# Optimization experiments

Hardware: AMD Instinct MI355X
Metric: run time of the kernel (lower is better)

The kernel has to match this reference:

```python
import jax, jax.numpy as jnp
import numpy as np

D_MODEL = 1024
N_HEADS = 16
HEAD_DIM = D_MODEL // N_HEADS
SEQ_LEN = 2048
BATCH = 2
THETA = 10000.0


def _rope_tables(dim, seq_len, theta=THETA):
    freqs = 1.0 / theta ** (jnp.arange(0, dim, 2, dtype=jnp.float32) / dim)  # (dim/2,)
    t = jnp.arange(seq_len, dtype=jnp.float32)
    ang = jnp.outer(t, freqs)  # (S, dim/2)
    # interleave each freq twice to match the (-x_odd, x_even) rotation layout
    cos = jnp.repeat(jnp.cos(ang), 2, axis=-1)  # (S, dim)
    sin = jnp.repeat(jnp.sin(ang), 2, axis=-1)
    return cos, sin


def _apply_rope(x, cos, sin):
    # x: (B, S, H, D); cos/sin: (S, D)
    x_rot = jnp.stack([-x[..., 1::2], x[..., ::2]], axis=-1).reshape(x.shape)
    return x * cos[None, :, None, :] + x_rot * sin[None, :, None, :]


def setup_inputs() -> dict:
    key = jax.random.key(0)
    ks = jax.random.split(key, 9)
    s = 1.0 / np.sqrt(D_MODEL)
    return {
        "x": jax.random.normal(ks[0], (BATCH, SEQ_LEN, D_MODEL), dtype=jnp.float32),
        "wq": jax.random.normal(ks[1], (D_MODEL, D_MODEL), jnp.float32) * s,
        "bq": jnp.zeros((D_MODEL,), jnp.float32),
        "wk": jax.random.normal(ks[2], (D_MODEL, D_MODEL), jnp.float32) * s,
        "bk": jnp.zeros((D_MODEL,), jnp.float32),
        "wv": jax.random.normal(ks[3], (D_MODEL, D_MODEL), jnp.float32) * s,
        "bv": jnp.zeros((D_MODEL,), jnp.float32),
        "wo": jax.random.normal(ks[4], (D_MODEL, D_MODEL), jnp.float32) * s,
        "bo": jnp.zeros((D_MODEL,), jnp.float32),
    }


def reference(x, wq, bq, wk, bk, wv, bv, wo, bo):
    B, S, _ = x.shape
    cos, sin = _rope_tables(HEAD_DIM, S)
    # projections (torch Linear: x @ W^T + b)
    q = (x @ wq.T + bq).reshape(B, S, N_HEADS, HEAD_DIM)
    k = (x @ wk.T + bk).reshape(B, S, N_HEADS, HEAD_DIM)
    v = (x @ wv.T + bv).reshape(B, S, N_HEADS, HEAD_DIM)
    q = _apply_rope(q, cos, sin)
    k = _apply_rope(k, cos, sin)
    # attention: bhqd, bhkd -> bhqk
    scale = 1.0 / np.sqrt(HEAD_DIM)
    scores = jnp.einsum("bqhd,bkhd->bhqk", q, k) * scale
    attn = jax.nn.softmax(scores, axis=-1)
    out = jnp.einsum("bhqk,bkhd->bqhd", attn, v).reshape(B, S, D_MODEL)
    return out @ wo.T + bo
```

## Files before the change

### kernel.cpp

```cpp
#include <hip/hip_runtime.h>

typedef __attribute__((ext_vector_type(8))) __bf16 bf16x8;
typedef __attribute__((ext_vector_type(4))) __bf16 bf16x4;
typedef __attribute__((ext_vector_type(4))) float f32x4;
typedef __attribute__((ext_vector_type(16))) float f32x16;
typedef __attribute__((ext_vector_type(4))) int i32x4;
typedef __attribute__((ext_vector_type(4))) unsigned short ushort4v;

__device__ __forceinline__ unsigned short f2bf(float f) {
  unsigned u = __builtin_bit_cast(unsigned, f);
  u += 0x7fffu + ((u >> 16) & 1u);
  return (unsigned short)(u >> 16);
}

__device__ __forceinline__ unsigned cvt_pk_bf16(float lo, float hi) {
  unsigned r;
  asm("v_cvt_pk_bf16_f32 %0, %1, %2" : "=v"(r) : "v"(lo), "v"(hi));
  return r;
}

__device__ __forceinline__ void pl32swap(unsigned& a, unsigned& b) {
  asm("v_permlane32_swap_b32 %0, %1" : "+v"(a), "+v"(b));
}

__device__ __forceinline__ void gload16(const void* g, void* l) {
  __builtin_amdgcn_global_load_lds(
      (const __attribute__((address_space(1))) void*)g,
      (__attribute__((address_space(3))) void*)l, 16, 0, 0);
}

__global__ __launch_bounds__(256) void convert_k(
    const float* __restrict__ x, const float* __restrict__ wq,
    const float* __restrict__ wk, const float* __restrict__ wv,
    const float* __restrict__ wo,
    unsigned short* __restrict__ xb, unsigned short* __restrict__ wqkv,
    unsigned short* __restrict__ wob, float* cosT, float* sinT) {
  if (blockIdx.x >= 8192) {
    const int idx = (blockIdx.x - 8192) * 256 + threadIdx.x;
    const int s = idx >> 5, j = idx & 31;
    const float freq = powf(10000.f, -(float)(2 * j) * (1.f / 64.f));
    const float ang = (float)s * freq;
    cosT[idx] = cosf(ang);
    sinT[idx] = sinf(ang);
    return;
  }
  const size_t i = ((size_t)blockIdx.x * 256 + threadIdx.x) * 4;
  const float* src; unsigned short* dst; size_t off;
  if (i < 4194304)      { src = x;  dst = xb;              off = i; }
  else if (i < 5242880) { src = wq; dst = wqkv;            off = i - 4194304; }
  else if (i < 6291456) { src = wk; dst = wqkv + 1048576;  off = i - 5242880; }
  else if (i < 7340032) { src = wv; dst = wqkv + 2097152;  off = i - 6291456; }
  else                  { src = wo; dst = wob;             off = i - 7340032; }
  f32x4 v = *(const f32x4*)(src + off);
  ushort4v o;
  o[0] = f2bf(v[0]); o[1] = f2bf(v[1]); o[2] = f2bf(v[2]); o[3] = f2bf(v[3]);
  *(ushort4v*)(dst + off) = o;
}

template <int EPI>
__global__ __launch_bounds__(512) void gemm_bt_k(
    const unsigned short* __restrict__ A, const unsigned short* __restrict__ B,
    int M, int N, int K,
    unsigned short* __restrict__ Qr, unsigned short* __restrict__ Kr,
    unsigned short* __restrict__ Vt,
    const float* __restrict__ bq, const float* __restrict__ bk,
    const float* __restrict__ bvv,
    const float* __restrict__ cosT, const float* __restrict__ sinT,
    float* __restrict__ Cout, const float* __restrict__ bias) {
  __shared__ char smem[32768];
  const int t = threadIdx.x;
  const int wave = t >> 6, lane = t & 63;
  const int l15 = lane & 15, g = lane >> 4;
  const int cpx = (int)gridDim.x >> 3;
  const int wg = (blockIdx.x & 7) * cpx + (blockIdx.x >> 3);
  const int nt = N >> 7;
  const int mb = (wg / nt) << 7;
  const int nb = (wg % nt) << 7;
  const int wm = (wave >> 2) << 6;
  const int wn = (wave & 3) << 5;

  const f32x4 zv = {0.f, 0.f, 0.f, 0.f};
  f32x4 acc[4][2];
#pragma unroll
  for (int i = 0; i < 4; i++)
#pragma unroll
    for (int j = 0; j < 2; j++) acc[i][j] = zv;

  for (int kt = 0; kt < K; kt += 64) {
#pragma unroll
    for (int i = 0; i < 2; i++) {
      const int lin = t * 16 + i * 8192;
      const int r = lin >> 7;
      const int cb = (lin & 127) ^ ((r & 7) << 4);
      gload16((const char*)A + ((size_t)(mb + r) * K + kt) * 2 + cb,
              smem + i * 8192 + wave * 1024);
      gload16((const char*)B + ((size_t)(nb + r) * K + kt) * 2 + cb,
              smem + 16384 + i * 8192 + wave * 1024);
    }
    __syncthreads();

    bf16x8 af[4][2], bfr[2][2];
    const int sw = (l15 & 7) << 4;
#pragma unroll
    for (int mf = 0; mf < 4; mf++) {
      const int r = wm + mf * 16 + l15;
#pragma unroll
      for (int kf = 0; kf < 2; kf++)
        af[mf][kf] = *(const bf16x8*)(smem + r * 128 + ((kf * 64 + g * 16) ^ sw));
    }
#pragma unroll
    for (int nf = 0; nf < 2; nf++) {
      const int r2 = wn + nf * 16 + l15;
#pragma unroll
      for (int kf = 0; kf < 2; kf++)
        bfr[nf][kf] = *(const bf16x8*)(smem + 16384 + r2 * 128 + ((kf * 64 + g * 16) ^ sw));
    }
#pragma unroll
    for (int mf = 0; mf < 4; mf++)
#pragma unroll
      for (int nf = 0; nf < 2; nf++) {
        acc[mf][nf] = __builtin_amdgcn_mfma_f32_16x16x32_bf16(af[mf][0], bfr[nf][0], acc[mf][nf], 0, 0, 0);
        acc[mf][nf] = __builtin_amdgcn_mfma_f32_16x16x32_bf16(af[mf][1], bfr[nf][1], acc[mf][nf], 0, 0, 0);
      }
    __syncthreads();
  }

#pragma unroll
  for (int mf = 0; mf < 4; mf++) {
#pragma unroll
    for (int nf = 0; nf < 2; nf++) {
      const int row0 = mb + wm + mf * 16 + g * 4;
      const int col = nb + wn + nf * 16 + l15;
      if (EPI == 1) {
        const float bsv = bias[col];
#pragma unroll
        for (int r = 0; r < 4; r++)
          Cout[(size_t)(row0 + r) * N + col] = acc[mf][nf][r] + bsv;
      } else {
        const int region = col >> 10;
        const int cc = col & 1023;
        const int h = cc >> 6, d = cc & 63;
        const float bias_v = (region == 0 ? bq : (region == 1 ? bk : bvv))[cc];
        if (region < 2) {
          unsigned short* Ob = (region == 0 ? Qr : Kr);
          const float scl = (region == 0) ? 0.180336880111120425f : 1.0f;
#pragma unroll
          for (int r = 0; r < 4; r++) {
            const int row = row0 + r;
            const int s = row & 2047;
            const int b = row >> 11;
            const float v = acc[mf][nf][r] + bias_v;
            const float p = __shfl_xor(v, 1);
            const float c = cosT[s * 32 + (d >> 1)];
            const float sn = sinT[s * 32 + (d >> 1)];
            float o = (d & 1) ? (v * c + p * sn) : (v * c - p * sn);
            o *= scl;
            Ob[((size_t)(b * 16 + h) * 2048 + s) * 64 + d] = f2bf(o);
          }
        } else {
          ushort4v w;
#pragma unroll
          for (int r = 0; r < 4; r++) w[r] = f2bf(acc[mf][nf][r] + bias_v);
          const int s = row0 & 2047;
          const int b = row0 >> 11;
          *(ushort4v*)(Vt + ((size_t)(b * 16 + h) * 64 + d) * 2048 + s) = w;
        }
      }
    }
  }
}

__global__ __launch_bounds__(256, 4) void flash_k(
    const unsigned short* __restrict__ Qr, const unsigned short* __restrict__ Kr,
    const unsigned short* __restrict__ Vt, unsigned short* __restrict__ Op,
    float* __restrict__ Lp) {
  __shared__ char smem[32768];
  const int bid = blockIdx.x;
  const int bh = ((bid & 7) << 2) | ((bid >> 3) & 3);
  const int rest = bid >> 5;
  const int qt = rest & 15;
  const int ck = rest >> 4;
  const int kvb = ck << 10;
  const int t = threadIdx.x;
  const int wave = t >> 6, lane = t & 63;
  const int l31 = lane & 31, h32 = lane >> 5;
  const int q0 = qt * 128 + wave * 32;
  const unsigned short* Qb = Qr + ((size_t)bh * 2048 + q0) * 64;
  const char* Kb = (const char*)(Kr + (size_t)bh * 2048 * 64);
  const char* Vb = (const char*)(Vt + (size_t)bh * 64 * 2048);

  bf16x8 qB[4];
#pragma unroll
  for (int t4 = 0; t4 < 4; t4++)
    qB[t4] = *(const bf16x8*)(Qb + l31 * 64 + t4 * 16 + h32 * 8);

  const f32x16 z16 = {0,0,0,0,0,0,0,0,0,0,0,0,0,0,0,0};
  f32x16 ot0 = z16, ot1 = z16;
  float lsum = 0.f;
  const int swv = (l31 & 7) << 4;

#pragma unroll
  for (int i = 0; i < 2; i++) {
    const int lin = t * 16 + i * 4096;
    const int r = lin >> 7;
    const int cb = (lin & 127) ^ ((r & 7) << 4);
    gload16(Kb + (size_t)(kvb + r) * 128 + cb, smem + i * 4096 + wave * 1024);
    gload16(Vb + (size_t)r * 4096 + kvb * 2 + cb, smem + 8192 + i * 4096 + wave * 1024);
  }
  __syncthreads();

  for (int it = 0; it < 16; ++it) {
    const char* kb = smem + (it & 1) * 16384;
    const char* vbuf = kb + 8192;
    if (it < 15) {
      const int kvn = kvb + ((it + 1) << 6);
      char* kd = smem + ((it & 1) ^ 1) * 16384;
#pragma unroll
      for (int i = 0; i < 2; i++) {
        const int lin = t * 16 + i * 4096;
        const int r = lin >> 7;
        const int cb = (lin & 127) ^ ((r & 7) << 4);
        gload16(Kb + (size_t)(kvn + r) * 128 + cb, kd + i * 4096 + wave * 1024);
        gload16(Vb + (size_t)r * 4096 + kvn * 2 + cb, kd + 8192 + i * 4096 + wave * 1024);
      }
    }
    f32x16 st0 = z16, st1 = z16;
#pragma unroll
    for (int t4 = 0; t4 < 4; t4++) {
      const bf16x8 ka0 = *(const bf16x8*)(kb + l31 * 128 + ((t4 * 32 + h32 * 16) ^ swv));
      const bf16x8 ka1 = *(const bf16x8*)(kb + (32 + l31) * 128 + ((t4 * 32 + h32 * 16) ^ swv));
      st0 = __builtin_amdgcn_mfma_f32_32x32x16_bf16(ka0, qB[t4], st0, 0, 0, 0);
      st1 = __builtin_amdgcn_mfma_f32_32x32x16_bf16(ka1, qB[t4], st1, 0, 0, 0);
    }
    float ls0 = 0.f, ls1 = 0.f;
#pragma unroll
    for (int e = 0; e < 16; e++) {
      const float p0 = __builtin_amdgcn_exp2f(st0[e] - 16.0f);
      const float p1 = __builtin_amdgcn_exp2f(st1[e] - 16.0f);
      st0[e] = p0; st1[e] = p1;
      ls0 += p0; ls1 += p1;
    }
    lsum += ls0 + ls1;
#pragma unroll
    for (int tile = 0; tile < 2; tile++) {
      const f32x16& s = tile ? st1 : st0;
#pragma unroll
      for (int sg = 0; sg < 2; sg++) {
        unsigned b0 = cvt_pk_bf16(s[8 * sg + 0], s[8 * sg + 1]);
        unsigned b1 = cvt_pk_bf16(s[8 * sg + 2], s[8 * sg + 3]);
        unsigned b2 = cvt_pk_bf16(s[8 * sg + 4], s[8 * sg + 5]);
        unsigned b3 = cvt_pk_bf16(s[8 * sg + 6], s[8 * sg + 7]);
        pl32swap(b0, b2);
        pl32swap(b1, b3);
        const i32x4 bw = {(int)b0, (int)b1, (int)b2, (int)b3};
        const bf16x8 pb = __builtin_bit_cast(bf16x8, bw);
        const int kvbyte = tile * 64 + sg * 32 + h32 * 16;
        const bf16x8 va0 = *(const bf16x8*)(vbuf + l31 * 128 + (kvbyte ^ swv));
        const bf16x8 va1 = *(const bf16x8*)(vbuf + (32 + l31) * 128 + (kvbyte ^ swv));
        ot0 = __builtin_amdgcn_mfma_f32_32x32x16_bf16(va0, pb, ot0, 0, 0, 0);
        ot1 = __builtin_amdgcn_mfma_f32_32x32x16_bf16(va1, pb, ot1, 0, 0, 0);
      }
    }
    __syncthreads();
  }
  lsum += __shfl_xor(lsum, 32);
  const size_t obase = (((size_t)(ck * 32 + bh)) * 2048 + q0 + l31) * 64;
#pragma unroll
  for (int dt = 0; dt < 2; dt++) {
#pragma unroll
    for (int grp = 0; grp < 4; grp++) {
      bf16x4 w;
#pragma unroll
      for (int e = 0; e < 4; e++)
        w[e] = (__bf16)(dt ? ot1[grp * 4 + e] : ot0[grp * 4 + e]);
      *(bf16x4*)(Op + obase + dt * 32 + grp * 8 + 4 * h32) = w;
    }
  }
  if (lane < 32)
    Lp[((size_t)(ck * 32 + bh)) * 2048 + q0 + l31] = lsum;
}

__global__ __launch_bounds__(256) void reduce_k(
    const unsigned short* __restrict__ Op, const float* __restrict__ Lp,
    unsigned short* __restrict__ Oa) {
  const size_t o = ((size_t)blockIdx.x * 256 + threadIdx.x) * 8;
  const int d0 = (int)(o & 63);
  const int h  = (int)((o >> 6) & 15);
  const int s  = (int)((o >> 10) & 2047);
  const int b  = (int)(o >> 21);
  const size_t pi = (((size_t)(b * 16 + h)) * 2048 + s) * 64 + d0;
  const size_t li = ((size_t)(b * 16 + h)) * 2048 + s;
  const bf16x8 a = *(const bf16x8*)(Op + pi);
  const bf16x8 c = *(const bf16x8*)(Op + pi + 4194304);
  const float inv = 1.f / (Lp[li] + Lp[li + 65536]);
  bf16x8 w;
#pragma unroll
  for (int e = 0; e < 8; e++)
    w[e] = (__bf16)(((float)a[e] + (float)c[e]) * inv);
  *(bf16x8*)(Oa + o) = w;
}

extern "C" void kernel_launch(void* const* d_in, const int* in_sizes, int n_in,
                              void* d_out, int out_size, void* d_ws, size_t ws_size,
                              hipStream_t stream) {
  const float* x  = (const float*)d_in[0];
  const float* wq = (const float*)d_in[1];
  const float* bq = (const float*)d_in[2];
  const float* wk = (const float*)d_in[3];
  const float* bk = (const float*)d_in[4];
  const float* wv = (const float*)d_in[5];
  const float* bv = (const float*)d_in[6];
  const float* wo = (const float*)d_in[7];
  const float* bo = (const float*)d_in[8];
  float* out = (float*)d_out;
  char* ws = (char*)d_ws;

  unsigned short* xb    = (unsigned short*)(ws);
  unsigned short* wqkv  = (unsigned short*)(ws + 8388608);
  float* cosT           = (float*)(ws + 14680064);
  float* sinT           = (float*)(ws + 14942208);
  unsigned short* Opart = (unsigned short*)(ws);
  unsigned short* Qr    = (unsigned short*)(ws + 16777216);
  unsigned short* Oa    = (unsigned short*)(ws + 16777216);
  unsigned short* Kr    = (unsigned short*)(ws + 25165824);
  unsigned short* Vt    = (unsigned short*)(ws + 33554432);
  unsigned short* wob   = (unsigned short*)(ws + 41943040);
  float* Lpart          = (float*)(ws + 44040192);

  convert_k<<<dim3(8448), dim3(256), 0, stream>>>(x, wq, wk, wv, wo, xb, wqkv, wob, cosT, sinT);
  gemm_bt_k<0><<<dim3(32 * 24), dim3(512), 0, stream>>>(
      xb, wqkv, 4096, 3072, 1024, Qr, Kr, Vt, bq, bk, bv, cosT, sinT,
      (float*)nullptr, (const float*)nullptr);
  flash_k<<<dim3(1024), dim3(256), 0, stream>>>(Qr, Kr, Vt, Opart, Lpart);
  reduce_k<<<dim3(2048), dim3(256), 0, stream>>>(Opart, Lpart, Oa);
  gemm_bt_k<1><<<dim3(32 * 8), dim3(512), 0, stream>>>(
      Oa, wob, 4096, 1024, 1024,
      (unsigned short*)nullptr, (unsigned short*)nullptr, (unsigned short*)nullptr,
      (const float*)nullptr, (const float*)nullptr, (const float*)nullptr,
      cosT, sinT, out, bo);
}
```

Baseline: 119.2 us.

## Fuse split-KV partial reduction into output projection GEMM A-tile load

Removes the separate reduce kernel that combined the two flash-attention partial outputs and normalized by the summed softmax denominators. The output-projection GEMM now reads both partials and the L values directly while staging its A tile, combining and normalizing them in registers before writing to shared memory. This drops one launch and the write and re-read of the combined attention output. In exchange the A path uses synchronous vector loads plus arithmetic instead of async direct-to-LDS loads. Each partial element is also read once per N-tile block (8 times), not once.

```diff
diff --git a/kernel.cpp b/kernel.cpp
--- a/kernel.cpp
+++ b/kernel.cpp
@@ -66,7 +66,8 @@
     const float* __restrict__ bq, const float* __restrict__ bk,
     const float* __restrict__ bvv,
     const float* __restrict__ cosT, const float* __restrict__ sinT,
-    float* __restrict__ Cout, const float* __restrict__ bias) {
+    float* __restrict__ Cout, const float* __restrict__ bias,
+    const float* __restrict__ Lpar) {
   __shared__ char smem[32768];
   const int t = threadIdx.x;
   const int wave = t >> 6, lane = t & 63;
@@ -87,15 +88,37 @@
     for (int j = 0; j < 2; j++) acc[i][j] = zv;
 
   for (int kt = 0; kt < K; kt += 64) {
-#pragma unroll
-    for (int i = 0; i < 2; i++) {
-      const int lin = t * 16 + i * 8192;
-      const int r = lin >> 7;
-      const int cb = (lin & 127) ^ ((r & 7) << 4);
-      gload16((const char*)A + ((size_t)(mb + r) * K + kt) * 2 + cb,
-              smem + i * 8192 + wave * 1024);
-      gload16((const char*)B + ((size_t)(nb + r) * K + kt) * 2 + cb,
-              smem + 16384 + i * 8192 + wave * 1024);
+    if (EPI == 2) {
+      const int h = kt >> 6;
+      const size_t rowb = ((size_t)((mb >> 11) * 16 + h)) * 2048 + (mb & 2047);
+#pragma unroll
+      for (int i = 0; i < 2; i++) {
+        const int lin = t * 16 + i * 8192;
+        const int r = lin >> 7;
+        const int cb = (lin & 127) ^ ((r & 7) << 4);
+        const size_t row = rowb + r;
+        const bf16x8 a0 = *(const bf16x8*)((const char*)A + row * 128 + cb);
+        const bf16x8 a1 = *(const bf16x8*)((const char*)A + (row + 65536ull) * 128 + cb);
+        const float inv = 1.f / (Lpar[row] + Lpar[row + 65536]);
+        bf16x8 w;
+#pragma unroll
+        for (int e = 0; e < 8; e++)
+          w[e] = (__bf16)(((float)a0[e] + (float)a1[e]) * inv);
+        *(bf16x8*)(smem + lin) = w;
+        gload16((const char*)B + ((size_t)(nb + r) * K + kt) * 2 + cb,
+                smem + 16384 + i * 8192 + wave * 1024);
+      }
+    } else {
+#pragma unroll
+      for (int i = 0; i < 2; i++) {
+        const int lin = t * 16 + i * 8192;
+        const int r = lin >> 7;
+        const int cb = (lin & 127) ^ ((r & 7) << 4);
+        gload16((const char*)A + ((size_t)(mb + r) * K + kt) * 2 + cb,
+                smem + i * 8192 + wave * 1024);
+        gload16((const char*)B + ((size_t)(nb + r) * K + kt) * 2 + cb,
+                smem + 16384 + i * 8192 + wave * 1024);
+      }
     }
     __syncthreads();
 
@@ -131,7 +154,7 @@
     for (int nf = 0; nf < 2; nf++) {
       const int row0 = mb + wm + mf * 16 + g * 4;
       const int col = nb + wn + nf * 16 + l15;
-      if (EPI == 1) {
+      if (EPI != 0) {
         const float bsv = bias[col];
 #pragma unroll
         for (int r = 0; r < 4; r++)
@@ -280,26 +303,6 @@
     Lp[((size_t)(ck * 32 + bh)) * 2048 + q0 + l31] = lsum;
 }
 
-__global__ __launch_bounds__(256) void reduce_k(
-    const unsigned short* __restrict__ Op, const float* __restrict__ Lp,
-    unsigned short* __restrict__ Oa) {
-  const size_t o = ((size_t)blockIdx.x * 256 + threadIdx.x) * 8;
-  const int d0 = (int)(o & 63);
-  const int h  = (int)((o >> 6) & 15);
-  const int s  = (int)((o >> 10) & 2047);
-  const int b  = (int)(o >> 21);
-  const size_t pi = (((size_t)(b * 16 + h)) * 2048 + s) * 64 + d0;
-  const size_t li = ((size_t)(b * 16 + h)) * 2048 + s;
-  const bf16x8 a = *(const bf16x8*)(Op + pi);
-  const bf16x8 c = *(const bf16x8*)(Op + pi + 4194304);
-  const float inv = 1.f / (Lp[li] + Lp[li + 65536]);
-  bf16x8 w;
-#pragma unroll
-  for (int e = 0; e < 8; e++)
-    w[e] = (__bf16)(((float)a[e] + (float)c[e]) * inv);
-  *(bf16x8*)(Oa + o) = w;
-}
-
 extern "C" void kernel_launch(void* const* d_in, const int* in_sizes, int n_in,
                               void* d_out, int out_size, void* d_ws, size_t ws_size,
                               hipStream_t stream) {
@@ -321,7 +324,6 @@
   float* sinT           = (float*)(ws + 14942208);
   unsigned short* Opart = (unsigned short*)(ws);
   unsigned short* Qr    = (unsigned short*)(ws + 16777216);
-  unsigned short* Oa    = (unsigned short*)(ws + 16777216);
   unsigned short* Kr    = (unsigned short*)(ws + 25165824);
   unsigned short* Vt    = (unsigned short*)(ws + 33554432);
   unsigned short* wob   = (unsigned short*)(ws + 41943040);
@@ -330,12 +332,11 @@
   convert_k<<<dim3(8448), dim3(256), 0, stream>>>(x, wq, wk, wv, wo, xb, wqkv, wob, cosT, sinT);
   gemm_bt_k<0><<<dim3(32 * 24), dim3(512), 0, stream>>>(
       xb, wqkv, 4096, 3072, 1024, Qr, Kr, Vt, bq, bk, bv, cosT, sinT,
-      (float*)nullptr, (const float*)nullptr);
+      (float*)nullptr, (const float*)nullptr, (const float*)nullptr);
   flash_k<<<dim3(1024), dim3(256), 0, stream>>>(Qr, Kr, Vt, Opart, Lpart);
-  reduce_k<<<dim3(2048), dim3(256), 0, stream>>>(Opart, Lpart, Oa);
-  gemm_bt_k<1><<<dim3(32 * 8), dim3(512), 0, stream>>>(
-      Oa, wob, 4096, 1024, 1024,
+  gemm_bt_k<2><<<dim3(32 * 8), dim3(512), 0, stream>>>(
+      Opart, wob, 4096, 1024, 1024,
       (unsigned short*)nullptr, (unsigned short*)nullptr, (unsigned short*)nullptr,
       (const float*)nullptr, (const float*)nullptr, (const float*)nullptr,
-      cosT, sinT, out, bo);
-}
+      cosT, sinT, out, bo, Lpart);
+}
```

Measured after the change: 122.3 us. +2.6%, slower.

## Replace QKV projection GEMM with 256x256-tile double-buffered pipelined kernel

Applied to the files above, without the earlier changes.

Adds a new QKV projection kernel that uses 256x256 output tiles and 128KB of LDS double buffering. Global-to-LDS prefetch of the next k-step is interleaved with four MFMA phases per step, using explicit waitcnt, barriers and setprio. The larger tiles are meant to raise data reuse and hide load latency behind compute. In exchange the grid shrinks to 192 workgroups, fewer than the CU count, so some compute units may sit idle. The old templated GEMM keeps only the output-projection epilogue.

```diff
diff --git a/kernel.cpp b/kernel.cpp
--- a/kernel.cpp
+++ b/kernel.cpp
@@ -27,6 +27,11 @@
   __builtin_amdgcn_global_load_lds(
       (const __attribute__((address_space(1))) void*)g,
       (__attribute__((address_space(3))) void*)l, 16, 0, 0);
+}
+
+__device__ __forceinline__ void barrier_f() {
+  __builtin_amdgcn_s_barrier();
+  asm volatile("" ::: "memory");
 }
 
 __global__ __launch_bounds__(256) void convert_k(
@@ -55,6 +60,213 @@
   ushort4v o;
   o[0] = f2bf(v[0]); o[1] = f2bf(v[1]); o[2] = f2bf(v[2]); o[3] = f2bf(v[3]);
   *(ushort4v*)(dst + off) = o;
+}
+
+__device__ __forceinline__ void g256_stA(const unsigned short* A, int mb,
+                                         int kt, char* dbuf, int a, int t) {
+  const int row = a * 64 + (t >> 3);
+  const int cb = ((t & 7) * 16) ^ ((row & 7) << 4);
+  gload16((const char*)A + ((size_t)(mb + row) * 1024 + kt) * 2 + cb,
+          dbuf + a * 8192 + t * 16);
+}
+__device__ __forceinline__ void g256_stB(const unsigned short* B, int nb,
+                                         int kt, char* dbuf, int u, int v, int t) {
+  const int bu = (t >= 256) ? v : u;
+  const int tt = t & 255;
+  const int row = bu * 32 + (tt >> 3);
+  const int cb = ((tt & 7) * 16) ^ ((row & 7) << 4);
+  gload16((const char*)B + ((size_t)(nb + row) * 1024 + kt) * 2 + cb,
+          dbuf + 32768 + bu * 4096 + tt * 16);
+}
+
+template <bool PF>
+__device__ __forceinline__ void g256_kstep(
+    const unsigned short* __restrict__ A, const unsigned short* __restrict__ B,
+    int mb, int nb, int kt, char* smem, int l15, int g,
+    int wm, int wn, int t, f32x4 (&acc)[8][4]) {
+  const int d = (kt >> 6) & 1;
+  const char* Ab = smem + d * 65536;
+  const char* Bb = Ab + 32768;
+  char* sn = smem + (d ^ 1) * 65536;
+  const int kn = kt + 64;
+  const int sw = (l15 & 7) << 4;
+  bf16x8 af[4][2], bf[2][2];
+
+#pragma unroll
+  for (int mf = 0; mf < 4; mf++) {
+    const int r = wm + mf * 16 + l15;
+#pragma unroll
+    for (int kf = 0; kf < 2; kf++)
+      af[mf][kf] = *(const bf16x8*)(Ab + r * 128 + ((kf * 64 + g * 16) ^ sw));
+  }
+#pragma unroll
+  for (int nf = 0; nf < 2; nf++) {
+    const int r = wn + nf * 16 + l15;
+#pragma unroll
+    for (int kf = 0; kf < 2; kf++)
+      bf[nf][kf] = *(const bf16x8*)(Bb + r * 128 + ((kf * 64 + g * 16) ^ sw));
+  }
+  if (PF) { g256_stA(A, mb, kn, sn, 0, t); g256_stA(A, mb, kn, sn, 2, t); }
+  asm volatile("s_waitcnt lgkmcnt(0)" ::: "memory");
+  __builtin_amdgcn_sched_barrier(0);
+  __builtin_amdgcn_s_setprio(1);
+#pragma unroll
+  for (int mf = 0; mf < 4; mf++)
+#pragma unroll
+    for (int nf = 0; nf < 2; nf++) {
+      acc[mf][nf] = __builtin_amdgcn_mfma_f32_16x16x32_bf16(af[mf][0], bf[nf][0], acc[mf][nf], 0, 0, 0);
+      acc[mf][nf] = __builtin_amdgcn_mfma_f32_16x16x32_bf16(af[mf][1], bf[nf][1], acc[mf][nf], 0, 0, 0);
+    }
+  __builtin_amdgcn_s_setprio(0);
+  if (PF) { asm volatile("s_waitcnt vmcnt(4)" ::: "memory"); }
+  else    { asm volatile("s_waitcnt vmcnt(2)" ::: "memory"); }
+  barrier_f();
+
+#pragma unroll
+  for (int nf = 0; nf < 2; nf++) {
+    const int r = wn + 32 + nf * 16 + l15;
+#pragma unroll
+    for (int kf = 0; kf < 2; kf++)
+      bf[nf][kf] = *(const bf16x8*)(Bb + r * 128 + ((kf * 64 + g * 16) ^ sw));
+  }
+  if (PF) { g256_stB(B, nb, kn, sn, 0, 2, t); g256_stB(B, nb, kn, sn, 4, 6, t); }
+  asm volatile("s_waitcnt lgkmcnt(0)" ::: "memory");
+  __builtin_amdgcn_sched_barrier(0);
+  __builtin_amdgcn_s_setprio(1);
+#pragma unroll
+  for (int mf = 0; mf < 4; mf++)
+#pragma unroll
+    for (int nf = 0; nf < 2; nf++) {
+      acc[mf][2 + nf] = __builtin_amdgcn_mfma_f32_16x16x32_bf16(af[mf][0], bf[nf][0], acc[mf][2 + nf], 0, 0, 0);
+      acc[mf][2 + nf] = __builtin_amdgcn_mfma_f32_16x16x32_bf16(af[mf][1], bf[nf][1], acc[mf][2 + nf], 0, 0, 0);
+    }
+  __builtin_amdgcn_s_setprio(0);
+  if (PF) { asm volatile("s_waitcnt vmcnt(4)" ::: "memory"); }
+  else    { asm volatile("s_waitcnt vmcnt(0)" ::: "memory"); }
+  barrier_f();
+
+#pragma unroll
+  for (int mf = 0; mf < 4; mf++) {
+    const int r = wm + 64 + mf * 16 + l15;
+#pragma unroll
+    for (int kf = 0; kf < 2; kf++)
+      af[mf][kf] = *(const bf16x8*)(Ab + r * 128 + ((kf * 64 + g * 16) ^ sw));
+  }
+  if (PF) { g256_stB(B, nb, kn, sn, 1, 3, t); g256_stB(B, nb, kn, sn, 5, 7, t); }
+  asm volatile("s_waitcnt lgkmcnt(0)" ::: "memory");
+  __builtin_amdgcn_sched_barrier(0);
+  __builtin_amdgcn_s_setprio(1);
+#pragma unroll
+  for (int mf = 0; mf < 4; mf++)
+#pragma unroll
+    for (int nf = 0; nf < 2; nf++) {
+      acc[4 + mf][2 + nf] = __builtin_amdgcn_mfma_f32_16x16x32_bf16(af[mf][0], bf[nf][0], acc[4 + mf][2 + nf], 0, 0, 0);
+      acc[4 + mf][2 + nf] = __builtin_amdgcn_mfma_f32_16x16x32_bf16(af[mf][1], bf[nf][1], acc[4 + mf][2 + nf], 0, 0, 0);
+    }
+  __builtin_amdgcn_s_setprio(0);
+  barrier_f();
+
+#pragma unroll
+  for (int nf = 0; nf < 2; nf++) {
+    const int r = wn + nf * 16 + l15;
+#pragma unroll
+    for (int kf = 0; kf < 2; kf++)
+      bf[nf][kf] = *(const bf16x8*)(Bb + r * 128 + ((kf * 64 + g * 16) ^ sw));
+  }
+  if (PF) { g256_stA(A, mb, kn, sn, 1, t); g256_stA(A, mb, kn, sn, 3, t); }
+  asm volatile("s_waitcnt lgkmcnt(0)" ::: "memory");
+  __builtin_amdgcn_sched_barrier(0);
+  __builtin_amdgcn_s_setprio(1);
+#pragma unroll
+  for (int mf = 0; mf < 4; mf++)
+#pragma unroll
+    for (int nf = 0; nf < 2; nf++) {
+      acc[4 + mf][nf] = __builtin_amdgcn_mfma_f32_16x16x32_bf16(af[mf][0], bf[nf][0], acc[4 + mf][nf], 0, 0, 0);
+      acc[4 + mf][nf] = __builtin_amdgcn_mfma_f32_16x16x32_bf16(af[mf][1], bf[nf][1], acc[4 + mf][nf], 0, 0, 0);
+    }
+  __builtin_amdgcn_s_setprio(0);
+  if (PF) {
+    asm volatile("s_waitcnt vmcnt(4)" ::: "memory");
+    barrier_f();
+  }
+}
+
+__global__ __launch_bounds__(512, 2) void gemm256_k(
+    const unsigned short* __restrict__ A, const unsigned short* __restrict__ B,
+    unsigned short* __restrict__ Qr, unsigned short* __restrict__ Kr,
+    unsigned short* __restrict__ Vt,
+    const float* __restrict__ bq, const float* __restrict__ bk,
+    const float* __restrict__ bvv,
+    const float* __restrict__ cosT, const float* __restrict__ sinT) {
+  __shared__ char smem[131072];
+  const int t = threadIdx.x;
+  const int wave = t >> 6, lane = t & 63;
+  const int l15 = lane & 15, g = lane >> 4;
+  const int cpx = (int)gridDim.x >> 3;
+  const int wg = (blockIdx.x & 7) * cpx + (blockIdx.x >> 3);
+  const int mb = (wg / 12) << 8;
+  const int nb = (wg % 12) << 8;
+  const int wm = (wave >> 2) << 7;
+  const int wn = (wave & 3) << 6;
+
+  const f32x4 zv = {0.f, 0.f, 0.f, 0.f};
+  f32x4 acc[8][4];
+#pragma unroll
+  for (int i = 0; i < 8; i++)
+#pragma unroll
+    for (int j = 0; j < 4; j++) acc[i][j] = zv;
+
+  g256_stA(A, mb, 0, smem, 0, t);
+  g256_stA(A, mb, 0, smem, 2, t);
+  g256_stB(B, nb, 0, smem, 0, 2, t);
+  g256_stB(B, nb, 0, smem, 4, 6, t);
+  g256_stB(B, nb, 0, smem, 1, 3, t);
+  g256_stB(B, nb, 0, smem, 5, 7, t);
+  g256_stA(A, mb, 0, smem, 1, t);
+  g256_stA(A, mb, 0, smem, 3, t);
+  asm volatile("s_waitcnt vmcnt(4)" ::: "memory");
+  barrier_f();
+
+  for (int kt = 0; kt < 960; kt += 64)
+    g256_kstep<true>(A, B, mb, nb, kt, smem, l15, g, wm, wn, t, acc);
+  g256_kstep<false>(A, B, mb, nb, 960, smem, l15, g, wm, wn, t, acc);
+
+#pragma unroll
+  for (int MF = 0; MF < 8; MF++) {
+#pragma unroll
+    for (int NF = 0; NF < 4; NF++) {
+      const int row0 = mb + wm + MF * 16 + g * 4;
+      const int col = nb + wn + NF * 16 + l15;
+      const int region = col >> 10;
+      const int cc = col & 1023;
+      const int h = cc >> 6, dd = cc & 63;
+      const float bias_v = (region == 0 ? bq : (region == 1 ? bk : bvv))[cc];
+      if (region < 2) {
+        unsigned short* Ob = (region == 0 ? Qr : Kr);
+        const float scl = (region == 0) ? 0.180336880111120425f : 1.0f;
+#pragma unroll
+        for (int r = 0; r < 4; r++) {
+          const int row = row0 + r;
+          const int s = row & 2047;
+          const int b = row >> 11;
+          const float v = acc[MF][NF][r] + bias_v;
+          const float p = __shfl_xor(v, 1);
+          const float c = cosT[s * 32 + (dd >> 1)];
+          const float sn = sinT[s * 32 + (dd >> 1)];
+          float o = (dd & 1) ? (v * c + p * sn) : (v * c - p * sn);
+          o *= scl;
+          Ob[((size_t)(b * 16 + h) * 2048 + s) * 64 + dd] = f2bf(o);
+        }
+      } else {
+        ushort4v w;
+#pragma unroll
+        for (int r = 0; r < 4; r++) w[r] = f2bf(acc[MF][NF][r] + bias_v);
+        const int s = row0 & 2047;
+        const int b = row0 >> 11;
+        *(ushort4v*)(Vt + ((size_t)(b * 16 + h) * 64 + dd) * 2048 + s) = w;
+      }
+    }
+  }
 }
 
 template <int EPI>
@@ -131,41 +343,10 @@
     for (int nf = 0; nf < 2; nf++) {
       const int row0 = mb + wm + mf * 16 + g * 4;
       const int col = nb + wn + nf * 16 + l15;
-      if (EPI == 1) {
-        const float bsv = bias[col];
-#pragma unroll
-        for (int r = 0; r < 4; r++)
-          Cout[(size_t)(row0 + r) * N + col] = acc[mf][nf][r] + bsv;
-      } else {
-        const int region = col >> 10;
-        const int cc = col & 1023;
-        const int h = cc >> 6, d = cc & 63;
-        const float bias_v = (region == 0 ? bq : (region == 1 ? bk : bvv))[cc];
-        if (region < 2) {
-          unsigned short* Ob = (region == 0 ? Qr : Kr);
-          const float scl = (region == 0) ? 0.180336880111120425f : 1.0f;
-#pragma unroll
-          for (int r = 0; r < 4; r++) {
-            const int row = row0 + r;
-            const int s = row & 2047;
-            const int b = row >> 11;
-            const float v = acc[mf][nf][r] + bias_v;
-            const float p = __shfl_xor(v, 1);
-            const float c = cosT[s * 32 + (d >> 1)];
-            const float sn = sinT[s * 32 + (d >> 1)];
-            float o = (d & 1) ? (v * c + p * sn) : (v * c - p * sn);
-            o *= scl;
-            Ob[((size_t)(b * 16 + h) * 2048 + s) * 64 + d] = f2bf(o);
-          }
-        } else {
-          ushort4v w;
-#pragma unroll
-          for (int r = 0; r < 4; r++) w[r] = f2bf(acc[mf][nf][r] + bias_v);
-          const int s = row0 & 2047;
-          const int b = row0 >> 11;
-          *(ushort4v*)(Vt + ((size_t)(b * 16 + h) * 64 + d) * 2048 + s) = w;
-        }
-      }
+      const float bsv = bias[col];
+#pragma unroll
+      for (int r = 0; r < 4; r++)
+        Cout[(size_t)(row0 + r) * N + col] = acc[mf][nf][r] + bsv;
     }
   }
 }
@@ -328,9 +509,8 @@
   float* Lpart          = (float*)(ws + 44040192);
 
   convert_k<<<dim3(8448), dim3(256), 0, stream>>>(x, wq, wk, wv, wo, xb, wqkv, wob, cosT, sinT);
-  gemm_bt_k<0><<<dim3(32 * 24), dim3(512), 0, stream>>>(
-      xb, wqkv, 4096, 3072, 1024, Qr, Kr, Vt, bq, bk, bv, cosT, sinT,
-      (float*)nullptr, (const float*)nullptr);
+  gemm256_k<<<dim3(192), dim3(512), 0, stream>>>(
+      xb, wqkv, Qr, Kr, Vt, bq, bk, bv, cosT, sinT);
   flash_k<<<dim3(1024), dim3(256), 0, stream>>>(Qr, Kr, Vt, Opart, Lpart);
   reduce_k<<<dim3(2048), dim3(256), 0, stream>>>(Opart, Lpart, Oa);
   gemm_bt_k<1><<<dim3(32 * 8), dim3(512), 0, stream>>>(
```

After: 122.6 us. 1.03x slower.
